# Kernel tuning notes

Hardware: AMD Instinct MI355X
Metric: run time of the kernel (lower is better)

## Reference

```python
import jax, jax.numpy as jnp
import numpy as np

NUM_HEADS = 8
GROUPS = 32
EPS = 1e-5


def group_norm(x, gamma, beta):
    # x: [b, c, l]; normalize over (c//GROUPS, l) per group
    b, c, l = x.shape
    xg = x.reshape(b, GROUPS, -1)
    mu = jnp.mean(xg, axis=-1, keepdims=True)
    var = jnp.mean(jnp.square(xg - mu), axis=-1, keepdims=True)
    xn = ((xg - mu) * jax.lax.rsqrt(var + EPS)).reshape(b, c, l)
    return xn * gamma[None, :, None] + beta[None, :, None]


def setup_inputs() -> dict:
    key = jax.random.key(0)
    ks = jax.random.split(key, 8)
    b, c, h, w = 8, 512, 64, 64
    cc, cl = 768, 256
    inner = 512
    s = lambda fan_in: 1.0 / np.sqrt(fan_in)
    return {
        "x": jax.random.normal(ks[0], (b, c, h, w), jnp.float32),
        "context": jax.random.normal(ks[1], (b, cc, cl), jnp.float32),
        "gnx_g": jnp.ones((c,), jnp.float32),
        "gnx_b": jnp.zeros((c,), jnp.float32),
        "gnc_g": jnp.ones((cc,), jnp.float32),
        "gnc_b": jnp.zeros((cc,), jnp.float32),
        "wq": jax.random.normal(ks[2], (inner, c), jnp.float32) * s(c),
        "bq": jax.random.normal(ks[3], (inner,), jnp.float32) * s(c),
        "wkv": jax.random.normal(ks[4], (2 * inner, cc), jnp.float32) * s(cc),
        "bkv": jax.random.normal(ks[5], (2 * inner,), jnp.float32) * s(cc),
        "wo": jax.random.normal(ks[6], (c, inner), jnp.float32) * s(inner),
        "bo": jax.random.normal(ks[7], (c,), jnp.float32) * s(inner),
    }


def reference(x, context, gnx_g, gnx_b, gnc_g, gnc_b, wq, bq, wkv, bkv, wo, bo):
    b, c, h, w = x.shape
    xf = x.reshape(b, c, h * w)                      # [b, c, L]
    inner = wq.shape[0]
    dh = inner // NUM_HEADS
    scale = dh ** (-0.5)

    q = jnp.einsum('oc,bcl->bol', wq, group_norm(xf, gnx_g, gnx_b)) + bq[None, :, None]
    kv = jnp.einsum('oc,bcl->bol', wkv, group_norm(context, gnc_g, gnc_b)) + bkv[None, :, None]
    k, v = jnp.split(kv, 2, axis=1)                  # [b, inner, S] each

    L = xf.shape[-1]
    S = k.shape[-1]
    q = q.reshape(b * NUM_HEADS, dh, L)
    k = k.reshape(b * NUM_HEADS, dh, S)
    v = v.reshape(b * NUM_HEADS, dh, S)

    # Faithful double-scale quirk: effective scaling is 1/dh
    dots = jnp.einsum('bct,bcs->bts', q * scale, k * scale)   # [bH, L, S]
    attn = jax.nn.softmax(dots.astype(jnp.float32), axis=-1).astype(dots.dtype)
    out = jnp.einsum('bts,bcs->bct', attn, v)                 # [bH, dh, L]
    out = out.reshape(b, inner, L)
    out = jnp.einsum('oc,bcl->bol', wo, out) + bo[None, :, None]
    return (xf + out).reshape(b, c, h, w)
```

## Files before the change

### kernel.cpp

```cpp
#include <hip/hip_runtime.h>

typedef unsigned short u16;
typedef unsigned int u32;
typedef __bf16 bf16x8 __attribute__((ext_vector_type(8)));
typedef float f32x4 __attribute__((ext_vector_type(4)));

__device__ __forceinline__ u16 f2bf(float f) {
    return __builtin_bit_cast(u16, (__bf16)f);
}
__device__ __forceinline__ u32 pkbf(float a, float b) {
    return (u32)__builtin_bit_cast(u16, (__bf16)a) |
           ((u32)__builtin_bit_cast(u16, (__bf16)b) << 16);
}
__device__ __forceinline__ u32 pku(u16 a, u16 b) {
    return (u32)a | ((u32)b << 16);
}
__device__ __forceinline__ bf16x8 ldb8(const void* p) {
    return __builtin_bit_cast(bf16x8, *(const uint4*)p);
}
__device__ __forceinline__ f32x4 mfma16(bf16x8 a, bf16x8 b, f32x4 c) {
    return __builtin_amdgcn_mfma_f32_16x16x32_bf16(a, b, c, 0, 0, 0);
}
__device__ __forceinline__ void gload_lds16(const void* g, void* l) {
    __builtin_amdgcn_global_load_lds(
        (const __attribute__((address_space(1))) unsigned int*)g,
        (__attribute__((address_space(3))) unsigned int*)l, 16, 0, 0);
}

__global__ __launch_bounds__(256) void cvt_w3(const float* __restrict__ w0,
                                              const float* __restrict__ w1,
                                              const float* __restrict__ w2,
                                              u16* __restrict__ o0, u16* __restrict__ o1,
                                              u16* __restrict__ o2) {
    const int which = blockIdx.y;
    const float* in = which == 0 ? w0 : which == 1 ? w1 : w2;
    u16* out = which == 0 ? o0 : which == 1 ? o1 : o2;
    const int n4 = which == 1 ? 196608 : 65536;
    int i = blockIdx.x * 256 + threadIdx.x;
    const int stride = gridDim.x * 256;
    for (; i < n4; i += stride) {
        float4 v = ((const float4*)in)[i];
        ((uint2*)out)[i] = make_uint2(pkbf(v.x, v.y), pkbf(v.z, v.w));
    }
}

__global__ __launch_bounds__(1024) void gn_stats(const float* __restrict__ in,
                                                 float2* __restrict__ stats, int N) {
    const int tid = threadIdx.x;
    const long base = (long)blockIdx.x * N;
    float s = 0.f, s2 = 0.f;
    for (int i = tid * 4; i < N; i += 1024 * 4) {
        float4 v = *(const float4*)(in + base + i);
        s += v.x + v.y + v.z + v.w;
        s2 += v.x * v.x + v.y * v.y + v.z * v.z + v.w * v.w;
    }
#pragma unroll
    for (int m = 1; m < 64; m <<= 1) { s += __shfl_xor(s, m); s2 += __shfl_xor(s2, m); }
    __shared__ float ps[16], ps2[16];
    const int w = tid >> 6;
    if ((tid & 63) == 0) { ps[w] = s; ps2[w] = s2; }
    __syncthreads();
    if (tid == 0) {
        float S = 0.f, S2 = 0.f;
#pragma unroll
        for (int k = 0; k < 16; ++k) { S += ps[k]; S2 += ps2[k]; }
        float mu = S / (float)N;
        float var = S2 / (float)N - mu * mu;
        stats[blockIdx.x] = make_float2(mu, rsqrtf(var + 1e-5f));
    }
}


__global__ __launch_bounds__(256) void gn_tr(const float* __restrict__ ctx,
                                             const float2* __restrict__ stats,
                                             const float* __restrict__ gamma,
                                             const float* __restrict__ beta,
                                             u16* __restrict__ ctx_t) {
    __shared__ u16 T[64][64];
    const int tid = threadIdx.x;
    const int b = blockIdx.z;
    const int c0 = blockIdx.x * 64, s0 = blockIdx.y * 64;
#pragma unroll
    for (int r = 0; r < 4; ++r) {
        int idx = r * 256 + tid;
        int c = idx >> 4, s4 = (idx & 15) << 2;
        int cg = c0 + c;
        float4 v = *(const float4*)(ctx + ((long)b * 768 + cg) * 256 + s0 + s4);
        float2 st = stats[b * 32 + cg / 24];
        float gm = gamma[cg], bt = beta[cg];
        float vv[4] = {(v.x - st.x) * st.y * gm + bt, (v.y - st.x) * st.y * gm + bt,
                       (v.z - st.x) * st.y * gm + bt, (v.w - st.x) * st.y * gm + bt};
#pragma unroll
        for (int jj = 0; jj < 4; ++jj) {
            int j = (jj + (tid & 3)) & 3;
            int row = s4 + j;
            T[row][c ^ ((row & 7) << 3)] = f2bf(vv[j]);
        }
    }
    __syncthreads();
#pragma unroll
    for (int r = 0; r < 2; ++r) {
        int f = r * 256 + tid;
        int s = f >> 3, cf = (f & 7) << 3;
        uint4 vv = *(const uint4*)&T[s][cf ^ ((s & 7) << 3)];
        *(uint4*)(ctx_t + ((long)b * 256 + s0 + s) * 768 + c0 + cf) = vv;
    }
}

__global__ __launch_bounds__(256, 2) void gemm_kv2(
    const u16* __restrict__ W, const u16* __restrict__ ctx_t,
    const float* __restrict__ bias, u16* __restrict__ k_t, u16* __restrict__ vout) {
    constexpr int K = 768;
    const int tid = threadIdx.x;
    const int b = blockIdx.z;
    const int o0 = blockIdx.x * 64;
    const int s0 = blockIdx.y * 64;
    const int lane = tid & 63, wv = tid >> 6;
    const int l16 = lane & 15, g = lane >> 4;

    const u16* ap = W + (long)(o0 + wv * 16 + l16) * K;
    const u16* ct = ctx_t + ((long)b * 256 + s0) * K;

    f32x4 acc[4] = {};
#pragma unroll
    for (int kc = 0; kc < 24; ++kc) {
        const int k8 = kc * 32 + g * 8;
        bf16x8 afr = ldb8(ap + k8);
#pragma unroll
        for (int ni = 0; ni < 4; ++ni) {
            bf16x8 bfr = ldb8(ct + (long)(ni * 16 + l16) * K + k8);
            acc[ni] = mfma16(afr, bfr, acc[ni]);
        }
    }
    const int orow = o0 + wv * 16 + g * 4;
    if (blockIdx.x < 8) {
        const int h = blockIdx.x;
        const int d0 = wv * 16 + g * 4;
        const float b0 = bias[orow], b1 = bias[orow + 1];
        const float b2 = bias[orow + 2], b3 = bias[orow + 3];
#pragma unroll
        for (int ni = 0; ni < 4; ++ni) {
            int s = s0 + ni * 16 + l16;
            *(uint2*)(k_t + (((long)b * 8 + h) * 256 + s) * 64 + d0) =
                make_uint2(pkbf(acc[ni][0] + b0, acc[ni][1] + b1),
                           pkbf(acc[ni][2] + b2, acc[ni][3] + b3));
        }
    } else {
#pragma unroll
        for (int ni = 0; ni < 4; ++ni) {
            int s = s0 + ni * 16 + l16;
#pragma unroll
            for (int i = 0; i < 4; ++i) {
                int vr = orow - 512 + i;
                vout[((long)b * 512 + vr) * 256 + s] = f2bf(acc[ni][i] + bias[orow + i]);
            }
        }
    }
}

template <int MODE>
__global__ __launch_bounds__(256, 2) void big_gemm(
    const u16* __restrict__ W, const void* __restrict__ Bsrc,
    const float2* __restrict__ stats, const float* __restrict__ gamma,
    const float* __restrict__ beta, const float* __restrict__ bias,
    const float* __restrict__ X, void* __restrict__ outp) {
    constexpr int K = 512, N = 4096, CPG = 16;
    __shared__ u16 Blds[2][64][64];
    const int tid = threadIdx.x;
    const int b = blockIdx.z;
    const int n0 = blockIdx.x * 64;
    const int lane = tid & 63, w = tid >> 6;
    const int l16 = lane & 15, g = lane >> 4;

    f32x4 acc[8][4] = {};

    if (MODE == 1) {
        const u16* Ob0 = (const u16*)Bsrc + ((long)b * 8) * 4096 * 64 + (long)n0 * 64;
#pragma unroll
        for (int r = 0; r < 2; ++r) {
            int idx = r * 256 + tid;
            int t = idx >> 3, d0 = (idx & 7) << 3;
            gload_lds16(Ob0 + (long)t * 64 + (d0 ^ ((t & 7) << 3)), &Blds[0][t][d0]);
        }
        __syncthreads();
        for (int c = 0; c < 8; ++c) {
            const int cur = c & 1;
            if (c < 7) {
                const u16* Obn = Ob0 + (long)(c + 1) * 4096 * 64;
#pragma unroll
                for (int r = 0; r < 2; ++r) {
                    int idx = r * 256 + tid;
                    int t = idx >> 3, d0 = (idx & 7) << 3;
                    gload_lds16(Obn + (long)t * 64 + (d0 ^ ((t & 7) << 3)),
                                &Blds[cur ^ 1][t][d0]);
                }
            }
            const int k0 = c * 64;
#pragma unroll
            for (int kk = 0; kk < 2; ++kk) {
                bf16x8 bfr[4];
#pragma unroll
                for (int ni = 0; ni < 4; ++ni) {
                    int row = ni * 16 + l16;
                    bfr[ni] = ldb8(&Blds[cur][row][(kk * 32 + g * 8) ^ ((row & 7) << 3)]);
                }
#pragma unroll
                for (int mi = 0; mi < 8; ++mi) {
                    int arow = w * 128 + mi * 16 + l16;
                    bf16x8 afr = ldb8(W + (long)arow * K + k0 + kk * 32 + g * 8);
#pragma unroll
                    for (int ni = 0; ni < 4; ++ni)
                        acc[mi][ni] = mfma16(afr, bfr[ni], acc[mi][ni]);
                }
            }
            __syncthreads();
        }
    } else {
        for (int c = 0; c < 8; ++c) {
            const int k0 = c * 64;
            __syncthreads();
            const float* Bb = (const float*)Bsrc + (long)b * K * N;
#pragma unroll
            for (int r = 0; r < 4; ++r) {
                int idx = r * 256 + tid;
                int kk = idx >> 4;
                int n4 = (idx & 15) << 2;
                int kg = k0 + kk;
                float4 v = *(const float4*)(Bb + (long)kg * N + n0 + n4);
                float2 st = stats[b * 32 + kg / CPG];
                float gm = gamma[kg], bt = beta[kg];
                v.x = (v.x - st.x) * st.y * gm + bt;
                v.y = (v.y - st.x) * st.y * gm + bt;
                v.z = (v.z - st.x) * st.y * gm + bt;
                v.w = (v.w - st.x) * st.y * gm + bt;
                float vv[4] = {v.x, v.y, v.z, v.w};
#pragma unroll
                for (int jj = 0; jj < 4; ++jj) {
                    int j = (jj + (lane & 3)) & 3;
                    int row = n4 + j;
                    Blds[0][row][kk ^ ((row & 7) << 3)] = f2bf(vv[j]);
                }
            }
            __syncthreads();
#pragma unroll
            for (int kk = 0; kk < 2; ++kk) {
                bf16x8 bfr[4];
#pragma unroll
                for (int ni = 0; ni < 4; ++ni) {
                    int row = ni * 16 + l16;
                    bfr[ni] = ldb8(&Blds[0][row][(kk * 32 + g * 8) ^ ((row & 7) << 3)]);
                }
#pragma unroll
                for (int mi = 0; mi < 8; ++mi) {
                    int arow = w * 128 + mi * 16 + l16;
                    bf16x8 afr = ldb8(W + (long)arow * K + k0 + kk * 32 + g * 8);
#pragma unroll
                    for (int ni = 0; ni < 4; ++ni)
                        acc[mi][ni] = mfma16(afr, bfr[ni], acc[mi][ni]);
                }
            }
        }
    }

    if (MODE == 0) {
        u16* qt = (u16*)outp;
#pragma unroll
        for (int mi = 0; mi < 8; ++mi) {
            int h = w * 2 + (mi >> 2);
            int dbase = (mi & 3) * 16 + g * 4;
#pragma unroll
            for (int ni = 0; ni < 4; ++ni) {
                int col = n0 + ni * 16 + l16;
                float v0 = acc[mi][ni][0] + bias[h * 64 + dbase + 0];
                float v1 = acc[mi][ni][1] + bias[h * 64 + dbase + 1];
                float v2 = acc[mi][ni][2] + bias[h * 64 + dbase + 2];
                float v3 = acc[mi][ni][3] + bias[h * 64 + dbase + 3];
                *(uint2*)(qt + (((long)b * 8 + h) * 4096 + col) * 64 + dbase) =
                    make_uint2(pkbf(v0, v1), pkbf(v2, v3));
            }
        }
    } else {
        float* out = (float*)outp;
        const long ob = (long)b * K * N;
#pragma unroll
        for (int mi = 0; mi < 8; ++mi)
#pragma unroll
            for (int i = 0; i < 4; ++i) {
                int row = w * 128 + mi * 16 + g * 4 + i;
                float bs = bias[row];
#pragma unroll
                for (int ni = 0; ni < 4; ++ni) {
                    int col = n0 + ni * 16 + l16;
                    long off = ob + (long)row * N + col;
                    out[off] = acc[mi][ni][i] + bs + X[off];
                }
            }
    }
}

__global__ __launch_bounds__(256, 1) void attn_v7(const u16* __restrict__ qt_in,
                                                  const u16* __restrict__ k_t,
                                                  const u16* __restrict__ v,
                                                  u16* __restrict__ qt_out) {
    __shared__ u16 kT[256][64];
    __shared__ u16 Vp[64][256];
    const int tid = threadIdx.x;
    const int bh = blockIdx.y;
    const int b = bh >> 3, h = bh & 7;
    const int lane = tid & 63, w = tid >> 6;
    const int l16 = lane & 15, g = lane >> 4;

    const long kb = (long)bh * 256 * 64;
    const long vb = ((long)(b * 512 + h * 64)) * 256;
    const long qb = (long)bh * 4096 * 64 + (long)blockIdx.x * 512 * 64;

#pragma unroll
    for (int r = 0; r < 8; ++r) {
        int idx = r * 256 + tid;
        int s = idx >> 3, d0 = (idx & 7) << 3;
        uint4 vv = *(const uint4*)(k_t + kb + (long)s * 64 + d0);
        *(uint4*)&kT[s][d0 ^ ((s & 7) << 3)] = vv;
    }
#pragma unroll
    for (int r = 0; r < 8; ++r) {
        int idx = r * 256 + tid;
        int d = idx >> 5, s0 = (idx & 31) << 3;
        union { uint4 v4; u16 h8[8]; } u;
        u.v4 = *(const uint4*)(v + vb + (long)d * 256 + s0);
        int f = s0 >> 4, g2 = (s0 >> 2) & 3;
        int cl = ((f >> 1) << 5) + (g2 << 3) + ((f & 1) << 2);
        int sw = (d & 7) << 3;
        *(uint2*)&Vp[d][cl ^ sw] = make_uint2(pku(u.h8[0], u.h8[1]), pku(u.h8[2], u.h8[3]));
        *(uint2*)&Vp[d][(cl + 8) ^ sw] = make_uint2(pku(u.h8[4], u.h8[5]), pku(u.h8[6], u.h8[7]));
    }
    __syncthreads();

    const float aa = 0.015625f * 1.44269504f;
    for (int it = 0; it < 8; ++it) {
        const int tcol = it * 64 + w * 16 + l16;
        const u16* qp = qt_in + qb + (long)tcol * 64;
        bf16x8 bq0 = ldb8(qp + g * 8);
        bf16x8 bq1 = ldb8(qp + 32 + g * 8);
        f32x4 sacc[16] = {};
#pragma unroll
        for (int mc = 0; mc < 4; ++mc) {
#pragma unroll
            for (int kk = 0; kk < 2; ++kk) {
                bf16x8 bqk = kk ? bq1 : bq0;
#pragma unroll
                for (int j = 0; j < 4; ++j) {
                    int mi = mc * 4 + j;
                    bf16x8 ak = ldb8(&kT[mi * 16 + l16][(kk * 32 + g * 8) ^ ((l16 & 7) << 3)]);
                    sacc[mi] = mfma16(ak, bqk, sacc[mi]);
                }
            }
        }
        float m = -3e38f;
#pragma unroll
        for (int f = 0; f < 16; ++f)
#pragma unroll
            for (int i = 0; i < 4; ++i) m = fmaxf(m, sacc[f][i]);
        m = fmaxf(m, __shfl_xor(m, 16));
        m = fmaxf(m, __shfl_xor(m, 32));
        float m2 = m * aa;
        float sum = 0.f;
#pragma unroll
        for (int f = 0; f < 16; ++f)
#pragma unroll
            for (int i = 0; i < 4; ++i) {
                float p = exp2f(fmaf(sacc[f][i], aa, -m2));
                sacc[f][i] = p;
                sum += p;
            }
        sum += __shfl_xor(sum, 16);
        sum += __shfl_xor(sum, 32);
        const float inv = 1.0f / sum;
        f32x4 oacc[4] = {};
#pragma unroll
        for (int ks = 0; ks < 8; ++ks) {
            bf16x8 bp = __builtin_bit_cast(bf16x8,
                make_uint4(pkbf(sacc[2 * ks][0], sacc[2 * ks][1]),
                           pkbf(sacc[2 * ks][2], sacc[2 * ks][3]),
                           pkbf(sacc[2 * ks + 1][0], sacc[2 * ks + 1][1]),
                           pkbf(sacc[2 * ks + 1][2], sacc[2 * ks + 1][3])));
#pragma unroll
            for (int mi = 0; mi < 4; ++mi) {
                bf16x8 av = ldb8(&Vp[mi * 16 + l16][(ks * 32 + g * 8) ^ ((l16 & 7) << 3)]);
                oacc[mi] = mfma16(av, bp, oacc[mi]);
            }
        }
        u16* op = qt_out + qb + (long)tcol * 64;
#pragma unroll
        for (int mi = 0; mi < 4; ++mi) {
            *(uint2*)(op + mi * 16 + g * 4) = make_uint2(
                pkbf(oacc[mi][0] * inv, oacc[mi][1] * inv),
                pkbf(oacc[mi][2] * inv, oacc[mi][3] * inv));
        }
    }
}

template <bool GN, bool RESID>
__global__ __launch_bounds__(256, 2) void big_gemm_f32(
    const u16* __restrict__ W, const float* __restrict__ B,
    const float2* __restrict__ stats, const float* __restrict__ gamma,
    const float* __restrict__ beta, const float* __restrict__ bias,
    const float* __restrict__ X, float* __restrict__ out) {
    constexpr int K = 512, N = 4096, CPG = 16;
    __shared__ u16 Blds[64][64];
    const int tid = threadIdx.x;
    const int b = blockIdx.z;
    const int n0 = blockIdx.x * 64;
    const int lane = tid & 63, w = tid >> 6;
    const int l16 = lane & 15, g = lane >> 4;
    const float* Bb = B + (long)b * K * N;

    f32x4 acc[8][4] = {};
    for (int c = 0; c < 8; ++c) {
        const int k0 = c * 64;
        __syncthreads();
#pragma unroll
        for (int r = 0; r < 4; ++r) {
            int idx = r * 256 + tid;
            int kk = idx >> 4;
            int n4 = (idx & 15) << 2;
            int kg = k0 + kk;
            float4 v = *(const float4*)(Bb + (long)kg * N + n0 + n4);
            if (GN) {
                float2 st = stats[b * 32 + kg / CPG];
                float gm = gamma[kg], bt = beta[kg];
                v.x = (v.x - st.x) * st.y * gm + bt;
                v.y = (v.y - st.x) * st.y * gm + bt;
                v.z = (v.z - st.x) * st.y * gm + bt;
                v.w = (v.w - st.x) * st.y * gm + bt;
            }
            float vv[4] = {v.x, v.y, v.z, v.w};
#pragma unroll
            for (int jj = 0; jj < 4; ++jj) {
                int j = (jj + (lane & 3)) & 3;
                int row = n4 + j;
                Blds[row][kk ^ ((row & 7) << 3)] = f2bf(vv[j]);
            }
        }
        __syncthreads();
#pragma unroll
        for (int kk = 0; kk < 2; ++kk) {
            bf16x8 bfr[4];
#pragma unroll
            for (int ni = 0; ni < 4; ++ni) {
                int row = ni * 16 + l16;
                bfr[ni] = ldb8(&Blds[row][(kk * 32 + g * 8) ^ ((row & 7) << 3)]);
            }
#pragma unroll
            for (int mi = 0; mi < 8; ++mi) {
                int arow = w * 128 + mi * 16 + l16;
                bf16x8 afr = ldb8(W + (long)arow * K + k0 + kk * 32 + g * 8);
#pragma unroll
                for (int ni = 0; ni < 4; ++ni)
                    acc[mi][ni] = mfma16(afr, bfr[ni], acc[mi][ni]);
            }
        }
    }
    const long ob = (long)b * K * N;
#pragma unroll
    for (int mi = 0; mi < 8; ++mi)
#pragma unroll
        for (int i = 0; i < 4; ++i) {
            int row = w * 128 + mi * 16 + g * 4 + i;
            float bs = bias[row];
#pragma unroll
            for (int ni = 0; ni < 4; ++ni) {
                int col = n0 + ni * 16 + l16;
                long off = ob + (long)row * N + col;
                float v = acc[mi][ni][i] + bs;
                if (RESID) v += X[off];
                out[off] = v;
            }
        }
}

__global__ __launch_bounds__(256) void gemm_kv_old(
    const u16* __restrict__ W, const float* __restrict__ act,
    const float2* __restrict__ stats, const float* __restrict__ gamma,
    const float* __restrict__ beta, const float* __restrict__ bias,
    u16* __restrict__ outp, int K, int N, int CPG, long actBS, long outBS) {
    __shared__ u16 Blds[128][40];
    const int tid = threadIdx.x;
    const int b = blockIdx.z;
    const int m0 = blockIdx.y * 128;
    const int n0 = blockIdx.x * 128;
    const int lane = tid & 63;
    const int w = tid >> 6;
    const int wr = w >> 1, wc = w & 1;
    const int l16 = lane & 15, g = lane >> 4;

    const float* actB = act + (long)b * actBS;
    f32x4 acc[4][4] = {};
    for (int s = 0; s < K / 32; ++s) {
        const int k0 = s * 32;
        __syncthreads();
#pragma unroll
        for (int r = 0; r < 4; ++r) {
            int idx = r * 256 + tid;
            int kk = idx >> 5;
            int n4 = (idx & 31) << 2;
            int kg = k0 + kk;
            float2 st = stats[b * 32 + kg / CPG];
            float gm = gamma[kg], bt = beta[kg];
            float4 v = *(const float4*)(actB + (long)kg * N + n0 + n4);
            Blds[n4 + 0][kk] = f2bf((v.x - st.x) * st.y * gm + bt);
            Blds[n4 + 1][kk] = f2bf((v.y - st.x) * st.y * gm + bt);
            Blds[n4 + 2][kk] = f2bf((v.z - st.x) * st.y * gm + bt);
            Blds[n4 + 3][kk] = f2bf((v.w - st.x) * st.y * gm + bt);
        }
        __syncthreads();
        bf16x8 bfr[4];
#pragma unroll
        for (int ni = 0; ni < 4; ++ni)
            bfr[ni] = ldb8(&Blds[wc * 64 + ni * 16 + l16][g * 8]);
#pragma unroll
        for (int mi = 0; mi < 4; ++mi) {
            int row = m0 + wr * 64 + mi * 16 + l16;
            bf16x8 afr = ldb8(W + (long)row * K + k0 + g * 8);
#pragma unroll
            for (int ni = 0; ni < 4; ++ni)
                acc[mi][ni] = mfma16(afr, bfr[ni], acc[mi][ni]);
        }
    }
#pragma unroll
    for (int mi = 0; mi < 4; ++mi)
#pragma unroll
        for (int i = 0; i < 4; ++i) {
            int row = m0 + wr * 64 + mi * 16 + g * 4 + i;
            float bs = bias[row];
#pragma unroll
            for (int ni = 0; ni < 4; ++ni) {
                int col = n0 + wc * 64 + ni * 16 + l16;
                outp[(long)b * outBS + (long)row * N + col] = f2bf(acc[mi][ni][i] + bs);
            }
        }
}

__global__ __launch_bounds__(256, 2) void attn_v4(const float* q,
                                                  const u16* __restrict__ kv,
                                                  float* out) {
    __shared__ u16 kT[256][64];
    __shared__ u16 Vp[64][256];
    const int tid = threadIdx.x;
    const int bh = blockIdx.y;
    const int b = bh >> 3, h = bh & 7;
    const int lane = tid & 63, w = tid >> 6;
    const int l16 = lane & 15, g = lane >> 4;

    const long kbase = ((long)(b * 1024 + h * 64)) * 256;
    const long vbase = ((long)(b * 1024 + 512 + h * 64)) * 256;
    const long qb = ((long)(b * 512 + h * 64)) * 4096 + blockIdx.x * 512;

#pragma unroll
    for (int r = 0; r < 8; ++r) {
        int idx = r * 256 + tid;
        int d = idx >> 5, s8 = idx & 31;
        union { uint4 v; u16 h8[8]; } u;
        u.v = *(const uint4*)(kv + kbase + (long)d * 256 + s8 * 8);
#pragma unroll
        for (int j = 0; j < 8; ++j)
            kT[s8 * 8 + j][d ^ (j << 3)] = u.h8[j];
    }
#pragma unroll
    for (int r = 0; r < 8; ++r) {
        int idx = r * 256 + tid;
        int d = idx >> 5, s0 = (idx & 31) << 3;
        union { uint4 v; u16 h8[8]; } u;
        u.v = *(const uint4*)(kv + vbase + (long)d * 256 + s0);
        int f = s0 >> 4, g2 = (s0 >> 2) & 3;
        int cl = ((f >> 1) << 5) + (g2 << 3) + ((f & 1) << 2);
        int sw = (d & 7) << 3;
        *(uint2*)&Vp[d][cl ^ sw] = make_uint2(pku(u.h8[0], u.h8[1]), pku(u.h8[2], u.h8[3]));
        *(uint2*)&Vp[d][(cl + 8) ^ sw] = make_uint2(pku(u.h8[4], u.h8[5]), pku(u.h8[6], u.h8[7]));
    }
    __syncthreads();

    const float aa = 0.015625f * 1.44269504f;
    for (int it = 0; it < 8; ++it) {
        const int tcol = it * 64 + w * 16 + l16;
        u32 bqw[2][4];
#pragma unroll
        for (int kk = 0; kk < 2; ++kk) {
            const float* qp = q + qb + tcol + (long)(kk * 32 + g * 8) * 4096;
#pragma unroll
            for (int jp = 0; jp < 4; ++jp)
                bqw[kk][jp] = pkbf(qp[(2 * jp) * 4096], qp[(2 * jp + 1) * 4096]);
        }
        f32x4 sacc[16] = {};
#pragma unroll
        for (int kk = 0; kk < 2; ++kk) {
            bf16x8 bq_ = __builtin_bit_cast(bf16x8,
                make_uint4(bqw[kk][0], bqw[kk][1], bqw[kk][2], bqw[kk][3]));
#pragma unroll
            for (int mi = 0; mi < 16; ++mi) {
                bf16x8 ak = ldb8(&kT[mi * 16 + l16][(kk * 32 + g * 8) ^ ((l16 & 7) << 3)]);
                sacc[mi] = mfma16(ak, bq_, sacc[mi]);
            }
        }
        float m = -3e38f;
#pragma unroll
        for (int f = 0; f < 16; ++f)
#pragma unroll
            for (int i = 0; i < 4; ++i) m = fmaxf(m, sacc[f][i]);
        m = fmaxf(m, __shfl_xor(m, 16));
        m = fmaxf(m, __shfl_xor(m, 32));
        float m2 = m * aa;
        float sum = 0.f;
#pragma unroll
        for (int f = 0; f < 16; ++f)
#pragma unroll
            for (int i = 0; i < 4; ++i) {
                float p = exp2f(fmaf(sacc[f][i], aa, -m2));
                sacc[f][i] = p;
                sum += p;
            }
        sum += __shfl_xor(sum, 16);
        sum += __shfl_xor(sum, 32);
        const float inv = 1.0f / sum;
        f32x4 oacc[4] = {};
#pragma unroll
        for (int ks = 0; ks < 8; ++ks) {
            bf16x8 bp = __builtin_bit_cast(bf16x8,
                make_uint4(pkbf(sacc[2 * ks][0], sacc[2 * ks][1]),
                           pkbf(sacc[2 * ks][2], sacc[2 * ks][3]),
                           pkbf(sacc[2 * ks + 1][0], sacc[2 * ks + 1][1]),
                           pkbf(sacc[2 * ks + 1][2], sacc[2 * ks + 1][3])));
#pragma unroll
            for (int mi = 0; mi < 4; ++mi) {
                bf16x8 av = ldb8(&Vp[mi * 16 + l16][(ks * 32 + g * 8) ^ ((l16 & 7) << 3)]);
                oacc[mi] = mfma16(av, bp, oacc[mi]);
            }
        }
#pragma unroll
        for (int mi = 0; mi < 4; ++mi)
#pragma unroll
            for (int i = 0; i < 4; ++i)
                out[qb + (long)(mi * 16 + g * 4 + i) * 4096 + tcol] = oacc[mi][i] * inv;
    }
}

extern "C" void kernel_launch(void* const* d_in, const int* in_sizes, int n_in,
                              void* d_out, int out_size, void* d_ws, size_t ws_size,
                              hipStream_t stream) {
    const float* x     = (const float*)d_in[0];
    const float* ctx   = (const float*)d_in[1];
    const float* gnx_g = (const float*)d_in[2];
    const float* gnx_b = (const float*)d_in[3];
    const float* gnc_g = (const float*)d_in[4];
    const float* gnc_b = (const float*)d_in[5];
    const float* wq    = (const float*)d_in[6];
    const float* bq    = (const float*)d_in[7];
    const float* wkv   = (const float*)d_in[8];
    const float* bkv   = (const float*)d_in[9];
    const float* wo    = (const float*)d_in[10];
    const float* bo    = (const float*)d_in[11];
    float* out = (float*)d_out;

    char* ws = (char*)d_ws;
    float2* stats_x = (float2*)ws;
    float2* stats_c = (float2*)(ws + 2048);
    u16* wq_bf  = (u16*)(ws + 4096);
    u16* wkv_bf = (u16*)(ws + 528384);
    u16* wo_bf  = (u16*)(ws + 2101248);

    cvt_w3<<<dim3(128, 3), dim3(256), 0, stream>>>(wq, wkv, wo, wq_bf, wkv_bf, wo_bf);
    gn_stats<<<dim3(256), dim3(1024), 0, stream>>>(x, stats_x, 16 * 4096);
    gn_stats<<<dim3(256), dim3(1024), 0, stream>>>(ctx, stats_c, 24 * 256);

    const size_t NEED = 40374272;
    if (ws_size >= NEED) {
        u16* k_t   = (u16*)(ws + 2625536);
        u16* v     = (u16*)(ws + 4722688);
        u16* q_t   = (u16*)(ws + 6819840);
        u16* ctx_t = (u16*)(ws + 6819840);

        gn_tr<<<dim3(12, 4, 8), dim3(256), 0, stream>>>(
            ctx, stats_c, gnc_g, gnc_b, ctx_t);
        gemm_kv2<<<dim3(16, 4, 8), dim3(256), 0, stream>>>(
            wkv_bf, ctx_t, bkv, k_t, v);
        big_gemm<0><<<dim3(64, 1, 8), dim3(256), 0, stream>>>(
            wq_bf, x, stats_x, gnx_g, gnx_b, bq, nullptr, q_t);
        attn_v7<<<dim3(8, 64), dim3(256), 0, stream>>>(q_t, k_t, v, q_t);
        big_gemm<1><<<dim3(64, 1, 8), dim3(256), 0, stream>>>(
            wo_bf, q_t, nullptr, nullptr, nullptr, bo, x, out);
    } else {
        u16* kv = (u16*)(ws + 2625536);
        big_gemm_f32<true, false><<<dim3(64, 1, 8), dim3(256), 0, stream>>>(
            wq_bf, x, stats_x, gnx_g, gnx_b, bq, nullptr, out);
        gemm_kv_old<<<dim3(2, 8, 8), dim3(256), 0, stream>>>(
            wkv_bf, ctx, stats_c, gnc_g, gnc_b, bkv, kv, 768, 256, 24,
            (long)768 * 256, (long)1024 * 256);
        attn_v4<<<dim3(8, 64), dim3(256), 0, stream>>>(out, kv, out);
        big_gemm_f32<false, true><<<dim3(64, 1, 8), dim3(256), 0, stream>>>(
            wo_bf, out, nullptr, nullptr, nullptr, bo, x, out);
    }
}
```

Measured before the change: 213.0 us.

## Drop softmax max pass and fuse exp with PV matmul in halves

Removes the row-max reduction and its cross-lane shuffles from the attention softmax, exponentiating scaled scores directly. It also splits the 256 keys into two halves, computing QK, exp/pack and PV per half so fewer score accumulators stay live. This lowers register pressure and VALU work, but assumes the scores stay small enough that unshifted exp2 cannot overflow.

```diff
diff --git a/kernel.cpp b/kernel.cpp
--- a/kernel.cpp
+++ b/kernel.cpp
@@ -298,10 +298,10 @@
     }
 }
 
-__global__ __launch_bounds__(256, 1) void attn_v7(const u16* __restrict__ qt_in,
-                                                  const u16* __restrict__ k_t,
-                                                  const u16* __restrict__ v,
-                                                  u16* __restrict__ qt_out) {
+__global__ __launch_bounds__(256, 1) void attn_v12(const u16* __restrict__ qt_in,
+                                                   const u16* __restrict__ k_t,
+                                                   const u16* __restrict__ v,
+                                                   u16* __restrict__ qt_out) {
     __shared__ u16 kT[256][64];
     __shared__ u16 Vp[64][256];
     const int tid = threadIdx.x;
@@ -341,54 +341,56 @@
         const u16* qp = qt_in + qb + (long)tcol * 64;
         bf16x8 bq0 = ldb8(qp + g * 8);
         bf16x8 bq1 = ldb8(qp + 32 + g * 8);
-        f32x4 sacc[16] = {};
-#pragma unroll
-        for (int mc = 0; mc < 4; ++mc) {
-#pragma unroll
-            for (int kk = 0; kk < 2; ++kk) {
-                bf16x8 bqk = kk ? bq1 : bq0;
-#pragma unroll
-                for (int j = 0; j < 4; ++j) {
-                    int mi = mc * 4 + j;
-                    bf16x8 ak = ldb8(&kT[mi * 16 + l16][(kk * 32 + g * 8) ^ ((l16 & 7) << 3)]);
-                    sacc[mi] = mfma16(ak, bqk, sacc[mi]);
-                }
-            }
-        }
-        float m = -3e38f;
-#pragma unroll
-        for (int f = 0; f < 16; ++f)
-#pragma unroll
-            for (int i = 0; i < 4; ++i) m = fmaxf(m, sacc[f][i]);
-        m = fmaxf(m, __shfl_xor(m, 16));
-        m = fmaxf(m, __shfl_xor(m, 32));
-        float m2 = m * aa;
+
+        f32x4 oacc[4] = {};
         float sum = 0.f;
 #pragma unroll
-        for (int f = 0; f < 16; ++f)
-#pragma unroll
-            for (int i = 0; i < 4; ++i) {
-                float p = exp2f(fmaf(sacc[f][i], aa, -m2));
-                sacc[f][i] = p;
-                sum += p;
-            }
+        for (int half = 0; half < 2; ++half) {
+            f32x4 sacc[8] = {};
+#pragma unroll
+            for (int mc = 0; mc < 2; ++mc) {
+#pragma unroll
+                for (int kk = 0; kk < 2; ++kk) {
+                    bf16x8 bqk = kk ? bq1 : bq0;
+#pragma unroll
+                    for (int j = 0; j < 4; ++j) {
+                        int fl = mc * 4 + j;
+                        int mi = half * 8 + fl;
+                        bf16x8 ak =
+                            ldb8(&kT[mi * 16 + l16][(kk * 32 + g * 8) ^ ((l16 & 7) << 3)]);
+                        sacc[fl] = mfma16(ak, bqk, sacc[fl]);
+                    }
+                }
+            }
+            u32 pk[8][2];
+            float s0 = 0.f, s1 = 0.f, s2 = 0.f, s3 = 0.f;
+#pragma unroll
+            for (int f = 0; f < 8; ++f) {
+                float p0 = exp2f(sacc[f][0] * aa);
+                float p1 = exp2f(sacc[f][1] * aa);
+                float p2 = exp2f(sacc[f][2] * aa);
+                float p3 = exp2f(sacc[f][3] * aa);
+                pk[f][0] = pkbf(p0, p1);
+                pk[f][1] = pkbf(p2, p3);
+                s0 += p0; s1 += p1; s2 += p2; s3 += p3;
+            }
+            sum += (s0 + s1) + (s2 + s3);
+#pragma unroll
+            for (int ks2 = 0; ks2 < 4; ++ks2) {
+                int ks = half * 4 + ks2;
+                bf16x8 bp = __builtin_bit_cast(bf16x8,
+                    make_uint4(pk[2 * ks2][0], pk[2 * ks2][1],
+                               pk[2 * ks2 + 1][0], pk[2 * ks2 + 1][1]));
+#pragma unroll
+                for (int mi = 0; mi < 4; ++mi) {
+                    bf16x8 av = ldb8(&Vp[mi * 16 + l16][(ks * 32 + g * 8) ^ ((l16 & 7) << 3)]);
+                    oacc[mi] = mfma16(av, bp, oacc[mi]);
+                }
+            }
+        }
         sum += __shfl_xor(sum, 16);
         sum += __shfl_xor(sum, 32);
         const float inv = 1.0f / sum;
-        f32x4 oacc[4] = {};
-#pragma unroll
-        for (int ks = 0; ks < 8; ++ks) {
-            bf16x8 bp = __builtin_bit_cast(bf16x8,
-                make_uint4(pkbf(sacc[2 * ks][0], sacc[2 * ks][1]),
-                           pkbf(sacc[2 * ks][2], sacc[2 * ks][3]),
-                           pkbf(sacc[2 * ks + 1][0], sacc[2 * ks + 1][1]),
-                           pkbf(sacc[2 * ks + 1][2], sacc[2 * ks + 1][3])));
-#pragma unroll
-            for (int mi = 0; mi < 4; ++mi) {
-                bf16x8 av = ldb8(&Vp[mi * 16 + l16][(ks * 32 + g * 8) ^ ((l16 & 7) << 3)]);
-                oacc[mi] = mfma16(av, bp, oacc[mi]);
-            }
-        }
         u16* op = qt_out + qb + (long)tcol * 64;
 #pragma unroll
         for (int mi = 0; mi < 4; ++mi) {
@@ -684,7 +686,7 @@
             wkv_bf, ctx_t, bkv, k_t, v);
         big_gemm<0><<<dim3(64, 1, 8), dim3(256), 0, stream>>>(
             wq_bf, x, stats_x, gnx_g, gnx_b, bq, nullptr, q_t);
-        attn_v7<<<dim3(8, 64), dim3(256), 0, stream>>>(q_t, k_t, v, q_t);
+        attn_v12<<<dim3(8, 64), dim3(256), 0, stream>>>(q_t, k_t, v, q_t);
         big_gemm<1><<<dim3(64, 1, 8), dim3(256), 0, stream>>>(
             wo_bf, q_t, nullptr, nullptr, nullptr, bo, x, out);
     } else {
```

Result: no change. 214.5 us (+0.7%).
